# Performance work log

Hardware: AMD Instinct MI355X
Metric: run time of the kernel (lower is better)

## Reference

```python
import jax, jax.numpy as jnp
import numpy as np

D = 768          # hidden_size
N_HEADS = 12
HEAD_DIM = D // N_HEADS  # 64
WINDOW = 128 // 2        # local_attention // 2 = 64 tokens each side
ROPE_THETA = 10000.0     # local_rope_theta


def _rope_freqs(T, dtype=jnp.float32):
    # complex rotation factors e^{i * pos * inv_freq}, shape [T, HEAD_DIM//2]
    inv_freq = 1.0 / (ROPE_THETA ** (jnp.arange(0, HEAD_DIM, 2, dtype=dtype) / HEAD_DIM))
    ang = jnp.arange(T, dtype=dtype)[:, None] * inv_freq[None, :]
    return jnp.exp(1j * ang.astype(jnp.complex64))


def _apply_rope(x, freqs):
    # x: [B, T, N, H]; split into (2, H//2) pairs as in the source reshape
    B, T, N, H = x.shape
    pairs = x.reshape(B, T, N, 2, H // 2)
    c = pairs[..., 0, :] + 1j * pairs[..., 1, :]          # [B,T,N,H//2]
    rot = c * freqs[None, :, None, :]                      # broadcast over B, heads
    out = jnp.stack([jnp.real(rot), jnp.imag(rot)], axis=-1)  # [B,T,N,H//2,2]
    return out.reshape(B, T, N, H)  # attention_scaling = 1.0 for default rope


def setup_inputs() -> dict:
    key = jax.random.key(0)
    k1, k2, k3 = jax.random.split(key, 3)
    B, T = 4, 2048
    hidden_states = jax.random.normal(k1, (B, T, D), dtype=jnp.float32)
    attention_mask = jnp.ones((B, T), dtype=jnp.int32)
    Wqkv = jax.random.normal(k2, (3 * D, D), dtype=jnp.float32) * (1.0 / np.sqrt(D))
    Wo = jax.random.normal(k3, (D, D), dtype=jnp.float32) * (1.0 / np.sqrt(D))
    return {"hidden_states": hidden_states, "attention_mask": attention_mask,
            "Wqkv": Wqkv, "Wo": Wo}


def reference(hidden_states, attention_mask, Wqkv, Wo):
    B, T, _ = hidden_states.shape
    # fused QKV projection (no bias in ModernBERT)
    qkv = jnp.einsum('btd,ed->bte', hidden_states, Wqkv)   # [B,T,3D]
    q, k, v = jnp.split(qkv, 3, axis=-1)
    to_heads = lambda x: x.reshape(B, T, N_HEADS, HEAD_DIM)
    q, k, v = to_heads(q), to_heads(k), to_heads(v)
    # rotary embedding (complex multiply)
    freqs = _rope_freqs(T)
    q = _apply_rope(q, freqs)
    k = _apply_rope(k, freqs)
    # sliding-window + padding mask
    pos = jnp.arange(T)
    window = jnp.abs(pos[:, None] - pos[None, :]) <= WINDOW   # [T,T]
    pad = attention_mask.astype(jnp.bool_)                    # [B,T]
    allowed = window[None, None, :, :] & pad[:, None, :, None] & pad[:, None, None, :]
    # eager SDPA
    scale = 1.0 / np.sqrt(HEAD_DIM)
    scores = jnp.einsum('bqnh,bknh->bnqk', q, k) * scale      # [B,N,T,T]
    scores = jnp.where(allowed, scores, jnp.finfo(scores.dtype).min)
    probs = jax.nn.softmax(scores, axis=-1)
    attn = jnp.einsum('bnqk,bknh->bqnh', probs, v)            # [B,T,N,H]
    attn = attn.reshape(B, T, D)
    return jnp.einsum('btd,ed->bte', attn, Wo)                # output proj
```

## Files before the change

kernel.cpp:

```cpp
#include <hip/hip_runtime.h>
#include <hip/hip_bf16.h>
#include <math.h>

#define BATCH 4
#define SEQ   2048
#define DMODEL 768
#define NHEADS 12
#define HDIM  64
#define WIN   64
#define QKV_LD 2304

typedef __attribute__((ext_vector_type(8))) short bf16x8;
typedef __attribute__((ext_vector_type(4))) float f32x4;

typedef __attribute__((address_space(1))) const unsigned int guint;
typedef __attribute__((address_space(3))) unsigned int luint;

__device__ inline void gl_lds16(const __hip_bfloat16* g, __hip_bfloat16* l) {
    __builtin_amdgcn_global_load_lds((guint*)g, (luint*)l, 16, 0, 0);
}

__device__ inline void to_out(float* p, float v) { *p = v; }
__device__ inline void to_out(__hip_bfloat16* p, float v) { *p = __float2bfloat16(v); }

#define N4_HID  (BATCH * SEQ * DMODEL / 4)
#define N4_WQKV (QKV_LD * DMODEL / 4)
#define N4_WO   (DMODEL * DMODEL / 4)
#define N_ROPE  (SEQ * 32)
#define SETUP_TOTAL (N4_HID + N4_WQKV + N4_WO + N_ROPE)

__device__ inline void cast4(const float* in, __hip_bfloat16* out, int i) {
    float4 v = ((const float4*)in)[i];
    union { ushort4 u; __hip_bfloat16 h[4]; } o;
    o.h[0] = __float2bfloat16(v.x); o.h[1] = __float2bfloat16(v.y);
    o.h[2] = __float2bfloat16(v.z); o.h[3] = __float2bfloat16(v.w);
    ((ushort4*)out)[i] = o.u;
}

__global__ __launch_bounds__(256) void setup_kernel(const float* __restrict__ hidden,
                                                    const float* __restrict__ Wqkv,
                                                    const float* __restrict__ Wo,
                                                    __hip_bfloat16* __restrict__ hid_bf,
                                                    __hip_bfloat16* __restrict__ wqkv_bf,
                                                    __hip_bfloat16* __restrict__ wo_bf,
                                                    float2* __restrict__ tab) {
    int id = blockIdx.x * 256 + threadIdx.x;
    if (id < N4_HID) {
        cast4(hidden, hid_bf, id);
    } else if (id < N4_HID + N4_WQKV) {
        cast4(Wqkv, wqkv_bf, id - N4_HID);
    } else if (id < N4_HID + N4_WQKV + N4_WO) {
        cast4(Wo, wo_bf, id - N4_HID - N4_WQKV);
    } else if (id < SETUP_TOTAL) {
        int idx = id - (N4_HID + N4_WQKV + N4_WO);
        int t = idx >> 5, j = idx & 31;
        const float L2T_OVER_32 = 13.287712379549449f / 32.0f;
        float inv = exp2f(-(float)j * L2T_OVER_32);
        float s, c;
        sincosf((float)t * inv, &s, &c);
        tab[idx] = make_float2(c, s);
    }
}

template <typename OutT, int NWN>
__global__ __launch_bounds__(256) void gemm_nt_bf16(const __hip_bfloat16* __restrict__ A,
                                                    const __hip_bfloat16* __restrict__ B,
                                                    OutT* __restrict__ C,
                                                    int lda, int ldb, int ldc, int K,
                                                    const float2* __restrict__ rope_tab) {
    constexpr int BN  = 64 * NWN;
    constexpr int NWM = 4 / NWN;
    constexpr int WM  = 128 / NWM;
    constexpr int MI  = WM / 16;

    __shared__ __align__(16) __hip_bfloat16 As[128 * 64];
    __shared__ __align__(16) __hip_bfloat16 Bs[BN * 64];

    const int tid  = threadIdx.x;
    const int lane = tid & 63;
    const int wave = tid >> 6;
    const int wm   = wave / NWN;
    const int wn   = wave % NWN;
    const int fr   = lane & 15;
    const int quad = lane >> 4;

    const int bid = blockIdx.x;
    const int x   = bid & 7;
    const int j   = bid >> 3;
    const int m0  = (x * 8 + (j & 7)) * 128;
    const int n0  = (j >> 3) * BN;

    f32x4 acc[MI][4];
#pragma unroll
    for (int i = 0; i < MI; i++)
#pragma unroll
        for (int jj = 0; jj < 4; jj++) acc[i][jj] = (f32x4){0.f, 0.f, 0.f, 0.f};

    for (int k0 = 0; k0 < K; k0 += 64) {
        __syncthreads();
#pragma unroll
        for (int c = 0; c < 4; c++) {
            int t = (wave * 4 + c) * 64 + lane;
            int row = t >> 3, ch = t & 7;
            int gcol = (ch ^ (row & 7)) * 8;
            gl_lds16(A + (size_t)(m0 + row) * lda + k0 + gcol, As + t * 8);
        }
#pragma unroll
        for (int c = 0; c < 2 * NWN; c++) {
            int t = (wave * 2 * NWN + c) * 64 + lane;
            int row = t >> 3, ch = t & 7;
            int gcol = (ch ^ (row & 7)) * 8;
            gl_lds16(B + (size_t)(n0 + row) * ldb + k0 + gcol, Bs + t * 8);
        }
        __syncthreads();

#pragma unroll
        for (int ks = 0; ks < 2; ks++) {
            bf16x8 af[MI], bf_[4];
#pragma unroll
            for (int mi = 0; mi < MI; mi++) {
                int row = wm * WM + mi * 16 + fr;
                int pos = (ks * 4 + quad) ^ (row & 7);
                af[mi] = *(const bf16x8*)(As + row * 64 + pos * 8);
            }
#pragma unroll
            for (int ni = 0; ni < 4; ni++) {
                int row = wn * 64 + ni * 16 + fr;
                int pos = (ks * 4 + quad) ^ (row & 7);
                bf_[ni] = *(const bf16x8*)(Bs + row * 64 + pos * 8);
            }
#pragma unroll
            for (int mi = 0; mi < MI; mi++)
#pragma unroll
                for (int ni = 0; ni < 4; ni++)
                    acc[mi][ni] = __builtin_amdgcn_mfma_f32_16x16x32_bf16(af[mi], bf_[ni], acc[mi][ni], 0, 0, 0);
        }
    }

    const int b0 = n0 + wn * 64;
    if (rope_tab != nullptr && b0 < 2 * DMODEL) {
#pragma unroll
        for (int mi = 0; mi < MI; mi++) {
#pragma unroll
            for (int r = 0; r < 4; r++) {
                int t = (m0 + wm * WM + mi * 16 + quad * 4 + r) & (SEQ - 1);
#pragma unroll
                for (int ni = 0; ni < 2; ni++) {
                    float2 cs = rope_tab[t * 32 + ni * 16 + fr];
                    float x0 = acc[mi][ni][r], x1 = acc[mi][ni + 2][r];
                    acc[mi][ni][r]     = x0 * cs.x - x1 * cs.y;
                    acc[mi][ni + 2][r] = x0 * cs.y + x1 * cs.x;
                }
            }
        }
    }

#pragma unroll
    for (int mi = 0; mi < MI; mi++)
#pragma unroll
        for (int ni = 0; ni < 4; ni++) {
            f32x4 v = acc[mi][ni];
            int gc = b0 + ni * 16 + fr;
            size_t rbase = (size_t)(m0 + wm * WM + mi * 16 + quad * 4);
#pragma unroll
            for (int r = 0; r < 4; r++)
                to_out(&C[(rbase + r) * ldc + gc], v[r]);
        }
}

#define PLD  192

__global__ __launch_bounds__(256) void attn_kernel(const __hip_bfloat16* __restrict__ qkv,
                                                   const int* __restrict__ mask,
                                                   __hip_bfloat16* __restrict__ attn) {
    __shared__ __align__(16) char smem[49152];
    __hip_bfloat16* Ks = (__hip_bfloat16*)smem;
    __hip_bfloat16* Pb = (__hip_bfloat16*)smem;
    __hip_bfloat16* Vt = (__hip_bfloat16*)(smem + 24576);

    const int tid  = threadIdx.x;
    const int lane = tid & 63;
    const int wave = tid >> 6;
    const int fr   = lane & 15;
    const int quad = lane >> 4;

    const int bid  = blockIdx.x;
    const int x    = bid & 7;
    const int j    = bid >> 3;
    const int b    = x >> 1;
    const int q0   = ((x & 1) * 16 + (j & 15)) * 64;
    const int head = j >> 4;

    const int klo = max(0, q0 - WIN);
    const int khi = min(SEQ, q0 + 64 + WIN);
    const int nk  = khi - klo;
    const int nt  = nk >> 4;
    const int nkc = nk >> 5;

    const size_t rowbase = (size_t)(b * SEQ) * QKV_LD + head * HDIM;

    for (int task = tid; task < nk * 8; task += 256) {
        int row = task >> 3, g = task & 7;
        uint4 v = *(const uint4*)(qkv + rowbase + (size_t)(klo + row) * QKV_LD + DMODEL + g * 8);
        *(uint4*)(Ks + row * 64 + (g ^ (row & 7)) * 8) = v;
    }
    {
        int h = lane;
        const __hip_bfloat16* vb = qkv + rowbase + 2 * DMODEL + h;
        int ng = nk >> 3;
        for (int g = wave; g < ng; g += 4) {
            unsigned int u0, u1, u2, u3;
            {
                unsigned short a0 = *(const unsigned short*)(vb + (size_t)(klo + g * 8 + 0) * QKV_LD);
                unsigned short a1 = *(const unsigned short*)(vb + (size_t)(klo + g * 8 + 1) * QKV_LD);
                unsigned short a2 = *(const unsigned short*)(vb + (size_t)(klo + g * 8 + 2) * QKV_LD);
                unsigned short a3 = *(const unsigned short*)(vb + (size_t)(klo + g * 8 + 3) * QKV_LD);
                unsigned short a4 = *(const unsigned short*)(vb + (size_t)(klo + g * 8 + 4) * QKV_LD);
                unsigned short a5 = *(const unsigned short*)(vb + (size_t)(klo + g * 8 + 5) * QKV_LD);
                unsigned short a6 = *(const unsigned short*)(vb + (size_t)(klo + g * 8 + 6) * QKV_LD);
                unsigned short a7 = *(const unsigned short*)(vb + (size_t)(klo + g * 8 + 7) * QKV_LD);
                u0 = (unsigned int)a0 | ((unsigned int)a1 << 16);
                u1 = (unsigned int)a2 | ((unsigned int)a3 << 16);
                u2 = (unsigned int)a4 | ((unsigned int)a5 << 16);
                u3 = (unsigned int)a6 | ((unsigned int)a7 << 16);
            }
            int cs = g ^ (h & 7);
            *(uint4*)(Vt + h * PLD + cs * 8) = make_uint4(u0, u1, u2, u3);
        }
    }

    const int qrow0 = q0 + wave * 16;
    bf16x8 aq0 = *(const bf16x8*)(qkv + rowbase + (size_t)(qrow0 + fr) * QKV_LD + quad * 8);
    bf16x8 aq1 = *(const bf16x8*)(qkv + rowbase + (size_t)(qrow0 + fr) * QKV_LD + 32 + quad * 8);

    const int* mb = mask + b * SEQ;
    int mq[4];
#pragma unroll
    for (int r = 0; r < 4; r++) mq[r] = mb[qrow0 + quad * 4 + r];

    __syncthreads();

    f32x4 sc[12];
#pragma unroll
    for (int kt = 0; kt < 12; kt++) sc[kt] = (f32x4){-1e30f, -1e30f, -1e30f, -1e30f};

#pragma unroll
    for (int kt = 0; kt < 12; kt++) {
        if (kt < nt) {
            int krow = kt * 16 + fr;
            int kg = klo + krow;
            int p0 = (quad) ^ (krow & 7);
            int p1 = (4 + quad) ^ (krow & 7);
            bf16x8 bk0 = *(const bf16x8*)(Ks + krow * 64 + p0 * 8);
            bf16x8 bk1 = *(const bf16x8*)(Ks + krow * 64 + p1 * 8);
            f32x4 a = (f32x4){0.f, 0.f, 0.f, 0.f};
            a = __builtin_amdgcn_mfma_f32_16x16x32_bf16(aq0, bk0, a, 0, 0, 0);
            a = __builtin_amdgcn_mfma_f32_16x16x32_bf16(aq1, bk1, a, 0, 0, 0);
            int mk = mb[kg];
            f32x4 s;
#pragma unroll
            for (int r = 0; r < 4; r++) {
                int qg = qrow0 + quad * 4 + r;
                bool ok = (abs(qg - kg) <= WIN) && (mk != 0) && (mq[r] != 0);
                s[r] = ok ? a[r] * 0.125f : -1e30f;
            }
            sc[kt] = s;
        }
    }

    f32x4 mx = sc[0];
#pragma unroll
    for (int kt = 1; kt < 12; kt++)
#pragma unroll
        for (int r = 0; r < 4; r++) mx[r] = fmaxf(mx[r], sc[kt][r]);
#pragma unroll
    for (int off = 8; off >= 1; off >>= 1)
#pragma unroll
        for (int r = 0; r < 4; r++) mx[r] = fmaxf(mx[r], __shfl_xor(mx[r], off));

    f32x4 sum = (f32x4){0.f, 0.f, 0.f, 0.f};
#pragma unroll
    for (int kt = 0; kt < 12; kt++)
#pragma unroll
        for (int r = 0; r < 4; r++) {
            float e = __expf(sc[kt][r] - mx[r]);
            sc[kt][r] = e;
            sum[r] += e;
        }
#pragma unroll
    for (int off = 8; off >= 1; off >>= 1)
#pragma unroll
        for (int r = 0; r < 4; r++) sum[r] += __shfl_xor(sum[r], off);
    f32x4 rs;
#pragma unroll
    for (int r = 0; r < 4; r++) rs[r] = 1.0f / sum[r];

    __syncthreads();
#pragma unroll
    for (int kt = 0; kt < 12; kt++) {
        if (kt < nt) {
#pragma unroll
            for (int r = 0; r < 4; r++) {
                int prow = wave * 16 + quad * 4 + r;
                int c = kt * 2 + (fr >> 3);
                int cs = c ^ (prow & 7);
                Pb[prow * PLD + cs * 8 + (fr & 7)] = __float2bfloat16(sc[kt][r] * rs[r]);
            }
        }
    }
    __syncthreads();

    f32x4 o[4];
#pragma unroll
    for (int ht = 0; ht < 4; ht++) o[ht] = (f32x4){0.f, 0.f, 0.f, 0.f};

#pragma unroll
    for (int kc = 0; kc < 6; kc++) {
        if (kc < nkc) {
            int cs = (kc * 4 + quad) ^ (fr & 7);
            bf16x8 ap = *(const bf16x8*)(Pb + (wave * 16 + fr) * PLD + cs * 8);
#pragma unroll
            for (int ht = 0; ht < 4; ht++) {
                bf16x8 bv = *(const bf16x8*)(Vt + (ht * 16 + fr) * PLD + cs * 8);
                o[ht] = __builtin_amdgcn_mfma_f32_16x16x32_bf16(ap, bv, o[ht], 0, 0, 0);
            }
        }
    }

    __hip_bfloat16* ob = attn + (size_t)(b * SEQ + qrow0) * DMODEL + head * HDIM;
#pragma unroll
    for (int r = 0; r < 4; r++)
#pragma unroll
        for (int ht = 0; ht < 4; ht++)
            ob[(size_t)(quad * 4 + r) * DMODEL + ht * 16 + fr] = __float2bfloat16(o[ht][r]);
}

extern "C" void kernel_launch(void* const* d_in, const int* in_sizes, int n_in,
                              void* d_out, int out_size, void* d_ws, size_t ws_size,
                              hipStream_t stream) {
    const float* hidden = (const float*)d_in[0];
    const int*   mask   = (const int*)d_in[1];
    const float* Wqkv   = (const float*)d_in[2];
    const float* Wo     = (const float*)d_in[3];
    float* out = (float*)d_out;

    char* w = (char*)d_ws;
    __hip_bfloat16* qkv_bf  = (__hip_bfloat16*)(w);
    __hip_bfloat16* hid_bf  = (__hip_bfloat16*)(w + 37748736);
    __hip_bfloat16* wqkv_bf = (__hip_bfloat16*)(w + 50331648);
    __hip_bfloat16* wo_bf   = (__hip_bfloat16*)(w + 53870592);
    __hip_bfloat16* attn_bf = (__hip_bfloat16*)(w + 55050240);
    float2*         tab     = (float2*)(w + 67633152);

    setup_kernel<<<SETUP_TOTAL / 256, 256, 0, stream>>>(hidden, Wqkv, Wo,
                                                        hid_bf, wqkv_bf, wo_bf, tab);

    gemm_nt_bf16<__hip_bfloat16, 2><<<18 * 64, 256, 0, stream>>>(hid_bf, wqkv_bf, qkv_bf,
                                                                 DMODEL, DMODEL, QKV_LD, DMODEL, tab);

    attn_kernel<<<(SEQ / 64) * NHEADS * BATCH, 256, 0, stream>>>(qkv_bf, mask, attn_bf);

    gemm_nt_bf16<float, 1><<<12 * 64, 256, 0, stream>>>(attn_bf, wo_bf, out,
                                                        DMODEL, DMODEL, DMODEL, DMODEL, nullptr);
}
```

Measured before the change: 183.3 us.

## Replace GEMM with 4-stage pipelined 512-thread kernel using async LDS loads

Rewrites the NT bf16 GEMM into a 512-thread, 128x128-tile kernel with a 4-buffer LDS ring. It prefetches three K-steps ahead, using explicit vmcnt waits and a single barrier per step, and raises wave priority around the MFMA block. The aim is to overlap global-to-LDS transfers with matrix math and drop the double sync per K-step. The output projection now uses 128-wide N tiles, which halves its grid to 384 blocks. The 128 KB LDS footprint limits occupancy to one block per CU, and the fewer blocks for the Wo GEMM may underfill the 256 CUs.

```diff
diff --git a/kernel.cpp b/kernel.cpp
--- a/kernel.cpp
+++ b/kernel.cpp
@@ -62,25 +62,21 @@
     }
 }
 
-template <typename OutT, int NWN>
-__global__ __launch_bounds__(256) void gemm_nt_bf16(const __hip_bfloat16* __restrict__ A,
-                                                    const __hip_bfloat16* __restrict__ B,
-                                                    OutT* __restrict__ C,
-                                                    int lda, int ldb, int ldc, int K,
-                                                    const float2* __restrict__ rope_tab) {
-    constexpr int BN  = 64 * NWN;
-    constexpr int NWM = 4 / NWN;
-    constexpr int WM  = 128 / NWM;
-    constexpr int MI  = WM / 16;
-
-    __shared__ __align__(16) __hip_bfloat16 As[128 * 64];
-    __shared__ __align__(16) __hip_bfloat16 Bs[BN * 64];
+template <typename OutT, bool ROPE>
+__global__ __launch_bounds__(512) void gemm_pipe(const __hip_bfloat16* __restrict__ A,
+                                                 const __hip_bfloat16* __restrict__ B,
+                                                 OutT* __restrict__ C,
+                                                 int lda, int ldb, int ldc,
+                                                 const float2* __restrict__ rope_tab) {
+    __shared__ __align__(16) char smem[131072];
+    __hip_bfloat16* As = (__hip_bfloat16*)smem;
+    __hip_bfloat16* Bs = (__hip_bfloat16*)(smem + 65536);
 
     const int tid  = threadIdx.x;
     const int lane = tid & 63;
     const int wave = tid >> 6;
-    const int wm   = wave / NWN;
-    const int wn   = wave % NWN;
+    const int wm   = wave >> 1;
+    const int wn   = wave & 1;
     const int fr   = lane & 15;
     const int quad = lane >> 4;
 
@@ -88,62 +84,76 @@
     const int x   = bid & 7;
     const int j   = bid >> 3;
     const int m0  = (x * 8 + (j & 7)) * 128;
-    const int n0  = (j >> 3) * BN;
-
-    f32x4 acc[MI][4];
-#pragma unroll
-    for (int i = 0; i < MI; i++)
+    const int n0  = (j >> 3) * 128;
+
+    f32x4 acc[2][4];
+#pragma unroll
+    for (int i = 0; i < 2; i++)
 #pragma unroll
         for (int jj = 0; jj < 4; jj++) acc[i][jj] = (f32x4){0.f, 0.f, 0.f, 0.f};
 
-    for (int k0 = 0; k0 < K; k0 += 64) {
-        __syncthreads();
-#pragma unroll
-        for (int c = 0; c < 4; c++) {
-            int t = (wave * 4 + c) * 64 + lane;
-            int row = t >> 3, ch = t & 7;
+    auto stage = [&](int t) {
+        const int s  = t & 3;
+        const int k0 = t * 64;
+#pragma unroll
+        for (int c = 0; c < 2; ++c) {
+            int tc  = c * 512 + tid;
+            int row = tc >> 3, ch = tc & 7;
             int gcol = (ch ^ (row & 7)) * 8;
-            gl_lds16(A + (size_t)(m0 + row) * lda + k0 + gcol, As + t * 8);
-        }
-#pragma unroll
-        for (int c = 0; c < 2 * NWN; c++) {
-            int t = (wave * 2 * NWN + c) * 64 + lane;
-            int row = t >> 3, ch = t & 7;
-            int gcol = (ch ^ (row & 7)) * 8;
-            gl_lds16(B + (size_t)(n0 + row) * ldb + k0 + gcol, Bs + t * 8);
-        }
-        __syncthreads();
-
-#pragma unroll
-        for (int ks = 0; ks < 2; ks++) {
-            bf16x8 af[MI], bf_[4];
-#pragma unroll
-            for (int mi = 0; mi < MI; mi++) {
-                int row = wm * WM + mi * 16 + fr;
+            gl_lds16(A + (size_t)(m0 + row) * lda + k0 + gcol, As + s * 8192 + tc * 8);
+            gl_lds16(B + (size_t)(n0 + row) * ldb + k0 + gcol, Bs + s * 8192 + tc * 8);
+        }
+    };
+
+    stage(0); stage(1); stage(2);
+
+#pragma unroll
+    for (int t = 0; t < 12; ++t) {
+        if (t < 10)       asm volatile("s_waitcnt vmcnt(8)" ::: "memory");
+        else if (t == 10) asm volatile("s_waitcnt vmcnt(4)" ::: "memory");
+        else              asm volatile("s_waitcnt vmcnt(0)" ::: "memory");
+        __builtin_amdgcn_s_barrier();
+        __builtin_amdgcn_sched_barrier(0);
+
+        if (t < 9) stage(t + 3);
+
+        const __hip_bfloat16* as = As + (t & 3) * 8192;
+        const __hip_bfloat16* bs = Bs + (t & 3) * 8192;
+        bf16x8 af[2][2], bfv[2][4];
+#pragma unroll
+        for (int ks = 0; ks < 2; ++ks) {
+#pragma unroll
+            for (int mi = 0; mi < 2; ++mi) {
+                int row = wm * 32 + mi * 16 + fr;
                 int pos = (ks * 4 + quad) ^ (row & 7);
-                af[mi] = *(const bf16x8*)(As + row * 64 + pos * 8);
-            }
-#pragma unroll
-            for (int ni = 0; ni < 4; ni++) {
+                af[ks][mi] = *(const bf16x8*)(as + row * 64 + pos * 8);
+            }
+#pragma unroll
+            for (int ni = 0; ni < 4; ++ni) {
                 int row = wn * 64 + ni * 16 + fr;
                 int pos = (ks * 4 + quad) ^ (row & 7);
-                bf_[ni] = *(const bf16x8*)(Bs + row * 64 + pos * 8);
-            }
-#pragma unroll
-            for (int mi = 0; mi < MI; mi++)
-#pragma unroll
-                for (int ni = 0; ni < 4; ni++)
-                    acc[mi][ni] = __builtin_amdgcn_mfma_f32_16x16x32_bf16(af[mi], bf_[ni], acc[mi][ni], 0, 0, 0);
-        }
+                bfv[ks][ni] = *(const bf16x8*)(bs + row * 64 + pos * 8);
+            }
+        }
+
+        __builtin_amdgcn_s_setprio(1);
+#pragma unroll
+        for (int ks = 0; ks < 2; ++ks)
+#pragma unroll
+            for (int mi = 0; mi < 2; ++mi)
+#pragma unroll
+                for (int ni = 0; ni < 4; ++ni)
+                    acc[mi][ni] = __builtin_amdgcn_mfma_f32_16x16x32_bf16(af[ks][mi], bfv[ks][ni], acc[mi][ni], 0, 0, 0);
+        __builtin_amdgcn_s_setprio(0);
     }
 
     const int b0 = n0 + wn * 64;
-    if (rope_tab != nullptr && b0 < 2 * DMODEL) {
-#pragma unroll
-        for (int mi = 0; mi < MI; mi++) {
+    if (ROPE && b0 < 2 * DMODEL) {
+#pragma unroll
+        for (int mi = 0; mi < 2; mi++) {
 #pragma unroll
             for (int r = 0; r < 4; r++) {
-                int t = (m0 + wm * WM + mi * 16 + quad * 4 + r) & (SEQ - 1);
+                int t = (m0 + wm * 32 + mi * 16 + quad * 4 + r) & (SEQ - 1);
 #pragma unroll
                 for (int ni = 0; ni < 2; ni++) {
                     float2 cs = rope_tab[t * 32 + ni * 16 + fr];
@@ -156,12 +166,12 @@
     }
 
 #pragma unroll
-    for (int mi = 0; mi < MI; mi++)
+    for (int mi = 0; mi < 2; mi++)
 #pragma unroll
         for (int ni = 0; ni < 4; ni++) {
             f32x4 v = acc[mi][ni];
             int gc = b0 + ni * 16 + fr;
-            size_t rbase = (size_t)(m0 + wm * WM + mi * 16 + quad * 4);
+            size_t rbase = (size_t)(m0 + wm * 32 + mi * 16 + quad * 4);
 #pragma unroll
             for (int r = 0; r < 4; r++)
                 to_out(&C[(rbase + r) * ldc + gc], v[r]);
@@ -355,11 +365,11 @@
     setup_kernel<<<SETUP_TOTAL / 256, 256, 0, stream>>>(hidden, Wqkv, Wo,
                                                         hid_bf, wqkv_bf, wo_bf, tab);
 
-    gemm_nt_bf16<__hip_bfloat16, 2><<<18 * 64, 256, 0, stream>>>(hid_bf, wqkv_bf, qkv_bf,
-                                                                 DMODEL, DMODEL, QKV_LD, DMODEL, tab);
+    gemm_pipe<__hip_bfloat16, true><<<18 * 64, 512, 0, stream>>>(hid_bf, wqkv_bf, qkv_bf,
+                                                                 DMODEL, DMODEL, QKV_LD, tab);
 
     attn_kernel<<<(SEQ / 64) * NHEADS * BATCH, 256, 0, stream>>>(qkv_bf, mask, attn_bf);
 
-    gemm_nt_bf16<float, 1><<<12 * 64, 256, 0, stream>>>(attn_bf, wo_bf, out,
-                                                        DMODEL, DMODEL, DMODEL, DMODEL, nullptr);
-}
+    gemm_pipe<float, false><<<6 * 64, 512, 0, stream>>>(attn_bf, wo_bf, out,
+                                                        DMODEL, DMODEL, DMODEL, nullptr);
+}
```

Result: faster. 170.3 us (-7.1%).
